# Optimization experiments

Hardware: AMD Instinct MI355X
Metric: run time of the kernel (lower is better)

The kernel has to match this reference:

```python
import jax, jax.numpy as jnp
import numpy as np

N = 131072      # octree nodes at this depth
C_IN = 256      # in_channels == out_channels
C_B = 64        # bottleneck channels = out_channels // 4
K = 27          # 3x3x3 octree kernel neighborhood
EPS = 1e-5


def _bn(x, g, b, m, v):
    # inference-style BatchNorm with given running stats
    return (x - m) * (g * jax.lax.rsqrt(v + EPS)) + b


def setup_inputs() -> dict:
    key = jax.random.key(0)
    ks = jax.random.split(key, 20)
    inp = {
        "data": jax.random.normal(ks[0], (N, C_IN), dtype=jnp.float32),
        "neigh": jax.random.randint(ks[1], (N, K), 0, N, dtype=jnp.int32),
        "depth": 6,
        # conv1x1a (Linear, no bias) + BN
        "w1": jax.random.normal(ks[2], (C_IN, C_B), dtype=jnp.float32) * 0.05,
        "bn1_g": jax.random.uniform(ks[3], (C_B,), dtype=jnp.float32) + 0.5,
        "bn1_b": jax.random.normal(ks[4], (C_B,), dtype=jnp.float32) * 0.1,
        "bn1_m": jax.random.normal(ks[5], (C_B,), dtype=jnp.float32) * 0.1,
        "bn1_v": jax.random.uniform(ks[6], (C_B,), dtype=jnp.float32) + 0.5,
        # octree conv3x3 (27-neighbor gather + GEMM, no bias) + BN
        "w3": jax.random.normal(ks[7], (K, C_B, C_B), dtype=jnp.float32) * 0.02,
        "bn2_g": jax.random.uniform(ks[8], (C_B,), dtype=jnp.float32) + 0.5,
        "bn2_b": jax.random.normal(ks[9], (C_B,), dtype=jnp.float32) * 0.1,
        "bn2_m": jax.random.normal(ks[10], (C_B,), dtype=jnp.float32) * 0.1,
        "bn2_v": jax.random.uniform(ks[11], (C_B,), dtype=jnp.float32) + 0.5,
        # conv1x1b + BN (no ReLU)
        "w2": jax.random.normal(ks[12], (C_B, C_IN), dtype=jnp.float32) * 0.05,
        "bn3_g": jax.random.uniform(ks[13], (C_IN,), dtype=jnp.float32) + 0.5,
        "bn3_b": jax.random.normal(ks[14], (C_IN,), dtype=jnp.float32) * 0.1,
        "bn3_m": jax.random.normal(ks[15], (C_IN,), dtype=jnp.float32) * 0.1,
        "bn3_v": jax.random.uniform(ks[16], (C_IN,), dtype=jnp.float32) + 0.5,
    }
    return inp


def reference(data, neigh, depth, w1, bn1_g, bn1_b, bn1_m, bn1_v,
              w3, bn2_g, bn2_b, bn2_m, bn2_v,
              w2, bn3_g, bn3_b, bn3_m, bn3_v):
    # conv1x1a + BN + ReLU
    c1 = jax.nn.relu(_bn(data @ w1, bn1_g, bn1_b, bn1_m, bn1_v))  # [N, C_B]
    # octree conv3x3: gather 27 neighbors then contract with [K, C_B, C_B]
    gathered = c1[neigh]                                          # [N, K, C_B]
    c2 = jnp.einsum('nkc,kcd->nd', gathered, w3)                  # [N, C_B]
    c2 = jax.nn.relu(_bn(c2, bn2_g, bn2_b, bn2_m, bn2_v))
    # conv1x1b + BN (no relu)
    c3 = _bn(c2 @ w2, bn3_g, bn3_b, bn3_m, bn3_v)                 # [N, C_IN]
    # residual (in_channels == out_channels -> identity shortcut) + ReLU
    return jax.nn.relu(c3 + data)
```

## Files before the change

### kernel.cpp

```cpp
#include <hip/hip_runtime.h>

#define NN 131072
#define CIN 256
#define CB 64
#define KNB 27

typedef __attribute__((ext_vector_type(8))) short short8_t;
typedef __attribute__((ext_vector_type(4))) float f32x4;

__device__ inline unsigned short f2bf(float f) {
    union { float f; unsigned u; } x; x.f = f;
    unsigned r = x.u + 0x7fffu + ((x.u >> 16) & 1u);
    return (unsigned short)(r >> 16);
}

__device__ inline f32x4 mfma16(short8_t a, short8_t b, f32x4 c) {
    return __builtin_amdgcn_mfma_f32_16x16x32_bf16(a, b, c, 0, 0, 0);
}

__global__ __launch_bounds__(256) void prep_kernel(
    const float* __restrict__ w1, const float* __restrict__ w3, const float* __restrict__ w2,
    const float* __restrict__ g1, const float* __restrict__ b1, const float* __restrict__ m1, const float* __restrict__ v1,
    const float* __restrict__ g2, const float* __restrict__ b2, const float* __restrict__ m2, const float* __restrict__ v2,
    const float* __restrict__ g3, const float* __restrict__ b3, const float* __restrict__ m3, const float* __restrict__ v3,
    unsigned short* __restrict__ w1p, unsigned short* __restrict__ w3p, unsigned short* __restrict__ w2p,
    float* __restrict__ bias1, float* __restrict__ bias2, float* __restrict__ bias3)
{
    int t = blockIdx.x * 256 + threadIdx.x;
    if (t < 16384) {
        int j = t & 7, lane = (t >> 3) & 63, tt = (t >> 9) & 3, s = t >> 11;
        int c = s * 32 + (lane >> 4) * 8 + j;
        int d = tt * 16 + (lane & 15);
        float sc = g1[d] * rsqrtf(v1[d] + 1e-5f);
        w1p[t] = f2bf(w1[c * CB + d] * sc);
    } else if (t < 16384 + 110592) {
        int u = t - 16384;
        int j = u & 7, lane = (u >> 3) & 63, tt = (u >> 9) & 3, s = (u >> 11) & 1, k = u >> 12;
        int c = s * 32 + (lane >> 4) * 8 + j;
        int d = tt * 16 + (lane & 15);
        float sc = g2[d] * rsqrtf(v2[d] + 1e-5f);
        w3p[u] = f2bf(w3[(k * CB + c) * CB + d] * sc);
    } else if (t < 143360) {
        int u = t - 126976;
        int j = u & 7, lane = (u >> 3) & 63, ct = (u >> 9) & 15, s = u >> 13;
        int c = s * 32 + (lane >> 4) * 8 + j;
        int d = ct * 16 + (lane & 15);
        float sc = g3[d] * rsqrtf(v3[d] + 1e-5f);
        w2p[u] = f2bf(w2[c * CIN + d] * sc);
    } else if (t < 143744) {
        int u = t - 143360;
        if (u < 64)       { float sc = g1[u] * rsqrtf(v1[u] + 1e-5f); bias1[u] = b1[u] - m1[u] * sc; }
        else if (u < 128) { int d = u - 64;  float sc = g2[d] * rsqrtf(v2[d] + 1e-5f); bias2[d] = b2[d] - m2[d] * sc; }
        else              { int d = u - 128; float sc = g3[d] * rsqrtf(v3[d] + 1e-5f); bias3[d] = b3[d] - m3[d] * sc; }
    }
}

__global__ __launch_bounds__(256) void k1_conv1x1a(
    const float* __restrict__ data, const unsigned short* __restrict__ w1p,
    const float* __restrict__ bias1, unsigned short* __restrict__ c1b)
{
    __shared__ short8_t w1s[2048];
    int tid = threadIdx.x;
    const short8_t* wsrc = (const short8_t*)w1p;
#pragma unroll
    for (int i = 0; i < 8; i++) w1s[tid + i * 256] = wsrc[tid + i * 256];

    int lane = tid & 63, wave = tid >> 6;
    int g = lane >> 4, r = lane & 15;
    int rowbase = blockIdx.x * 128 + wave * 32;
    f32x4 acc[2][4] = {};
    __syncthreads();

#pragma unroll
    for (int s = 0; s < 8; s++) {
        short8_t a[2];
#pragma unroll
        for (int sub = 0; sub < 2; sub++) {
            const float* ap = data + (size_t)(rowbase + sub * 16 + r) * CIN + s * 32 + g * 8;
            float4 f0 = *(const float4*)ap;
            float4 f1 = *(const float4*)(ap + 4);
            short8_t av;
            av[0] = (short)f2bf(f0.x); av[1] = (short)f2bf(f0.y);
            av[2] = (short)f2bf(f0.z); av[3] = (short)f2bf(f0.w);
            av[4] = (short)f2bf(f1.x); av[5] = (short)f2bf(f1.y);
            av[6] = (short)f2bf(f1.z); av[7] = (short)f2bf(f1.w);
            a[sub] = av;
        }
#pragma unroll
        for (int t = 0; t < 4; t++) {
            short8_t b = w1s[(s * 4 + t) * 64 + lane];
            acc[0][t] = mfma16(a[0], b, acc[0][t]);
            acc[1][t] = mfma16(a[1], b, acc[1][t]);
        }
    }

#pragma unroll
    for (int sub = 0; sub < 2; sub++)
#pragma unroll
        for (int t = 0; t < 4; t++) {
            int col = t * 16 + r;
            float bs = bias1[col];
#pragma unroll
            for (int i = 0; i < 4; i++) {
                int row = rowbase + sub * 16 + g * 4 + i;
                c1b[row * CB + col] = f2bf(fmaxf(acc[sub][t][i] + bs, 0.f));
            }
        }
}

__global__ __launch_bounds__(256) void k2_conv3x3(
    const unsigned short* __restrict__ c1b, const int* __restrict__ neigh,
    const unsigned short* __restrict__ w3p, const float* __restrict__ bias2,
    unsigned short* __restrict__ c2b)
{
    __shared__ short8_t w3s[512];
    int tid = threadIdx.x;
    int lane = tid & 63, wave = tid >> 6;
    int g = lane >> 4, r = lane & 15;
    int rowbase = blockIdx.x * 128 + wave * 32;
    int n0 = rowbase + r, n1 = rowbase + 16 + r;
    f32x4 acc[2][4] = {};

    for (int k = 0; k < KNB; k++) {
        __syncthreads();
        const short8_t* src = (const short8_t*)(w3p + k * 4096);
        w3s[tid]       = src[tid];
        w3s[tid + 256] = src[tid + 256];

        int idx0 = neigh[n0 * KNB + k];
        int idx1 = neigh[n1 * KNB + k];
        const short8_t* ap0 = (const short8_t*)(c1b + (size_t)idx0 * CB);
        const short8_t* ap1 = (const short8_t*)(c1b + (size_t)idx1 * CB);
        short8_t a0s0 = ap0[g], a0s1 = ap0[4 + g];
        short8_t a1s0 = ap1[g], a1s1 = ap1[4 + g];
        __syncthreads();

#pragma unroll
        for (int t = 0; t < 4; t++) {
            short8_t b0 = w3s[t * 64 + lane];
            short8_t b1 = w3s[(4 + t) * 64 + lane];
            acc[0][t] = mfma16(a0s0, b0, acc[0][t]);
            acc[1][t] = mfma16(a1s0, b0, acc[1][t]);
            acc[0][t] = mfma16(a0s1, b1, acc[0][t]);
            acc[1][t] = mfma16(a1s1, b1, acc[1][t]);
        }
    }

#pragma unroll
    for (int sub = 0; sub < 2; sub++)
#pragma unroll
        for (int t = 0; t < 4; t++) {
            int col = t * 16 + r;
            float bs = bias2[col];
#pragma unroll
            for (int i = 0; i < 4; i++) {
                int row = rowbase + sub * 16 + g * 4 + i;
                c2b[row * CB + col] = f2bf(fmaxf(acc[sub][t][i] + bs, 0.f));
            }
        }
}

__global__ __launch_bounds__(256) void k3_conv1x1b(
    const unsigned short* __restrict__ c2b, const unsigned short* __restrict__ w2p,
    const float* __restrict__ bias3, const float* __restrict__ data,
    float* __restrict__ out)
{
    __shared__ short8_t w2s[2048];
    int tid = threadIdx.x;
    const short8_t* wsrc = (const short8_t*)w2p;
#pragma unroll
    for (int i = 0; i < 8; i++) w2s[tid + i * 256] = wsrc[tid + i * 256];

    int lane = tid & 63, wave = tid >> 6;
    int g = lane >> 4, r = lane & 15;
    int rowbase = blockIdx.x * 64;

    short8_t a[4][2];
#pragma unroll
    for (int sub = 0; sub < 4; sub++) {
        const short8_t* ap = (const short8_t*)(c2b + (size_t)(rowbase + sub * 16 + r) * CB);
        a[sub][0] = ap[g];
        a[sub][1] = ap[4 + g];
    }
    f32x4 acc[4][4] = {};
    __syncthreads();

#pragma unroll
    for (int s = 0; s < 2; s++)
#pragma unroll
        for (int t = 0; t < 4; t++) {
            short8_t b = w2s[(s * 16 + wave * 4 + t) * 64 + lane];
#pragma unroll
            for (int sub = 0; sub < 4; sub++)
                acc[sub][t] = mfma16(a[sub][s], b, acc[sub][t]);
        }

#pragma unroll
    for (int sub = 0; sub < 4; sub++)
#pragma unroll
        for (int t = 0; t < 4; t++) {
            int col = (wave * 4 + t) * 16 + r;
            float bs = bias3[col];
#pragma unroll
            for (int i = 0; i < 4; i++) {
                int row = rowbase + sub * 16 + g * 4 + i;
                size_t o = (size_t)row * CIN + col;
                out[o] = fmaxf(acc[sub][t][i] + bs + data[o], 0.f);
            }
        }
}

extern "C" void kernel_launch(void* const* d_in, const int* in_sizes, int n_in,
                              void* d_out, int out_size, void* d_ws, size_t ws_size,
                              hipStream_t stream)
{
    const float* data = (const float*)d_in[0];
    const int* neigh  = (const int*)d_in[1];
    const float* w1 = (const float*)d_in[3];
    const float* g1 = (const float*)d_in[4];
    const float* b1 = (const float*)d_in[5];
    const float* m1 = (const float*)d_in[6];
    const float* v1 = (const float*)d_in[7];
    const float* w3 = (const float*)d_in[8];
    const float* g2 = (const float*)d_in[9];
    const float* b2 = (const float*)d_in[10];
    const float* m2 = (const float*)d_in[11];
    const float* v2 = (const float*)d_in[12];
    const float* w2 = (const float*)d_in[13];
    const float* g3 = (const float*)d_in[14];
    const float* b3 = (const float*)d_in[15];
    const float* m3 = (const float*)d_in[16];
    const float* v3 = (const float*)d_in[17];
    float* out = (float*)d_out;

    char* ws = (char*)d_ws;
    unsigned short* c1b = (unsigned short*)ws;
    unsigned short* c2b = (unsigned short*)(ws + 16777216);
    unsigned short* w1p = (unsigned short*)(ws + 33554432);
    unsigned short* w3p = (unsigned short*)(ws + 33554432 + 32768);
    unsigned short* w2p = (unsigned short*)(ws + 33554432 + 32768 + 221184);
    float* bias1 = (float*)(ws + 33554432 + 32768 + 221184 + 32768);
    float* bias2 = bias1 + 64;
    float* bias3 = bias1 + 128;

    int n = in_sizes[0] / CIN;

    hipLaunchKernelGGL(prep_kernel, dim3(562), dim3(256), 0, stream,
                       w1, w3, w2, g1, b1, m1, v1, g2, b2, m2, v2, g3, b3, m3, v3,
                       w1p, w3p, w2p, bias1, bias2, bias3);
    hipLaunchKernelGGL(k1_conv1x1a, dim3(n / 128), dim3(256), 0, stream, data, w1p, bias1, c1b);
    hipLaunchKernelGGL(k2_conv3x3,  dim3(n / 128), dim3(256), 0, stream, c1b, neigh, w3p, bias2, c2b);
    hipLaunchKernelGGL(k3_conv1x1b, dim3(n / 64),  dim3(256), 0, stream, c2b, w2p, bias3, data, out);
}
```

Baseline: 198.2 us.

## Software-pipeline conv3x3 gathers and coalesce conv1x1b residual epilogue via LDS

The 3x3 octree conv kernel now stages the block's neighbor indices in LDS once. It double-buffers the gathered activations and weight fragments in registers, loaded directly from global memory, so the loads for step k+1 overlap the MFMAs for step k and the two per-step barriers disappear. The conv1x1b kernel drops its LDS weight staging in favour of direct global loads, and routes its output through an LDS tile so the residual add and store use coalesced float4 accesses. The cost is higher register pressure in k2, which gets a launch-bounds occupancy hint, and more LDS use in k3.

After: 172.5 us. -13.0%, faster.

```diff
diff --git a/kernel.cpp b/kernel.cpp
--- a/kernel.cpp
+++ b/kernel.cpp
@@ -108,43 +108,69 @@
         }
 }
 
-__global__ __launch_bounds__(256) void k2_conv3x3(
+#define K2_MFMA(aX, bX) \
+    _Pragma("unroll") for (int t = 0; t < 4; t++) { \
+        acc[0][t] = mfma16(aX[0], bX[t],     acc[0][t]); \
+        acc[1][t] = mfma16(aX[2], bX[t],     acc[1][t]); \
+        acc[0][t] = mfma16(aX[1], bX[4 + t], acc[0][t]); \
+        acc[1][t] = mfma16(aX[3], bX[4 + t], acc[1][t]); \
+    }
+
+#define K2_BODY(aC, bC, ixC0, ixC1, aN, bN, ixN0, ixN1, k) \
+    { \
+        if ((k) < 26) { \
+            const short8_t* p0 = (const short8_t*)(c1b + (size_t)(ixN0) * CB); \
+            const short8_t* p1 = (const short8_t*)(c1b + (size_t)(ixN1) * CB); \
+            aN[0] = p0[g]; aN[1] = p0[4 + g]; aN[2] = p1[g]; aN[3] = p1[4 + g]; \
+            const short8_t* bp = bbase + ((k) + 1) * 512; \
+            _Pragma("unroll") for (int f = 0; f < 8; f++) bN[f] = bp[f * 64 + lane]; \
+        } \
+        if ((k) < 25) { ixC0 = nidx[lr0 * KNB + (k) + 2]; ixC1 = nidx[lr1 * KNB + (k) + 2]; } \
+        K2_MFMA(aC, bC) \
+    }
+
+__global__ __launch_bounds__(256, 3) void k2_conv3x3(
     const unsigned short* __restrict__ c1b, const int* __restrict__ neigh,
     const unsigned short* __restrict__ w3p, const float* __restrict__ bias2,
     unsigned short* __restrict__ c2b)
 {
-    __shared__ short8_t w3s[512];
+    __shared__ int nidx[128 * KNB];
     int tid = threadIdx.x;
+    int rowbase = blockIdx.x * 128;
+
+    const int4* nsrc = (const int4*)(neigh + (size_t)rowbase * KNB);
+#pragma unroll
+    for (int i = 0; i < 4; i++) {
+        int p = tid + i * 256;
+        if (p < 864) ((int4*)nidx)[p] = nsrc[p];
+    }
+
     int lane = tid & 63, wave = tid >> 6;
     int g = lane >> 4, r = lane & 15;
-    int rowbase = blockIdx.x * 128 + wave * 32;
-    int n0 = rowbase + r, n1 = rowbase + 16 + r;
+    int lr0 = wave * 32 + r, lr1 = lr0 + 16;
+    __syncthreads();
+
+    const short8_t* bbase = (const short8_t*)w3p;
     f32x4 acc[2][4] = {};
-
-    for (int k = 0; k < KNB; k++) {
-        __syncthreads();
-        const short8_t* src = (const short8_t*)(w3p + k * 4096);
-        w3s[tid]       = src[tid];
-        w3s[tid + 256] = src[tid + 256];
-
-        int idx0 = neigh[n0 * KNB + k];
-        int idx1 = neigh[n1 * KNB + k];
-        const short8_t* ap0 = (const short8_t*)(c1b + (size_t)idx0 * CB);
-        const short8_t* ap1 = (const short8_t*)(c1b + (size_t)idx1 * CB);
-        short8_t a0s0 = ap0[g], a0s1 = ap0[4 + g];
-        short8_t a1s0 = ap1[g], a1s1 = ap1[4 + g];
-        __syncthreads();
-
-#pragma unroll
-        for (int t = 0; t < 4; t++) {
-            short8_t b0 = w3s[t * 64 + lane];
-            short8_t b1 = w3s[(4 + t) * 64 + lane];
-            acc[0][t] = mfma16(a0s0, b0, acc[0][t]);
-            acc[1][t] = mfma16(a1s0, b0, acc[1][t]);
-            acc[0][t] = mfma16(a0s1, b1, acc[0][t]);
-            acc[1][t] = mfma16(a1s1, b1, acc[1][t]);
-        }
-    }
+    short8_t aA[4], aB[4], bA[8], bB[8];
+    int ixA0, ixA1, ixB0, ixB1;
+
+    ixA0 = nidx[lr0 * KNB + 0]; ixA1 = nidx[lr1 * KNB + 0];
+    ixB0 = nidx[lr0 * KNB + 1]; ixB1 = nidx[lr1 * KNB + 1];
+    {
+        const short8_t* p0 = (const short8_t*)(c1b + (size_t)ixA0 * CB);
+        const short8_t* p1 = (const short8_t*)(c1b + (size_t)ixA1 * CB);
+        aA[0] = p0[g]; aA[1] = p0[4 + g]; aA[2] = p1[g]; aA[3] = p1[4 + g];
+#pragma unroll
+        for (int f = 0; f < 8; f++) bA[f] = bbase[f * 64 + lane];
+    }
+
+    for (int kk = 0; kk < 13; kk++) {
+        int k0 = kk * 2;
+        K2_BODY(aA, bA, ixA0, ixA1, aB, bB, ixB0, ixB1, k0)
+        K2_BODY(aB, bB, ixB0, ixB1, aA, bA, ixA0, ixA1, k0 + 1)
+    }
+    K2_BODY(aA, bA, ixA0, ixA1, aB, bB, ixB0, ixB1, 26)
 
 #pragma unroll
     for (int sub = 0; sub < 2; sub++)
@@ -154,7 +180,7 @@
             float bs = bias2[col];
 #pragma unroll
             for (int i = 0; i < 4; i++) {
-                int row = rowbase + sub * 16 + g * 4 + i;
+                int row = rowbase + wave * 32 + sub * 16 + g * 4 + i;
                 c2b[row * CB + col] = f2bf(fmaxf(acc[sub][t][i] + bs, 0.f));
             }
         }
@@ -165,16 +191,13 @@
     const float* __restrict__ bias3, const float* __restrict__ data,
     float* __restrict__ out)
 {
-    __shared__ short8_t w2s[2048];
+    __shared__ float otile[64 * 260];
     int tid = threadIdx.x;
-    const short8_t* wsrc = (const short8_t*)w2p;
-#pragma unroll
-    for (int i = 0; i < 8; i++) w2s[tid + i * 256] = wsrc[tid + i * 256];
-
     int lane = tid & 63, wave = tid >> 6;
     int g = lane >> 4, r = lane & 15;
     int rowbase = blockIdx.x * 64;
 
+    const short8_t* bbase = (const short8_t*)w2p;
     short8_t a[4][2];
 #pragma unroll
     for (int sub = 0; sub < 4; sub++) {
@@ -183,13 +206,11 @@
         a[sub][1] = ap[4 + g];
     }
     f32x4 acc[4][4] = {};
-    __syncthreads();
-
 #pragma unroll
     for (int s = 0; s < 2; s++)
 #pragma unroll
         for (int t = 0; t < 4; t++) {
-            short8_t b = w2s[(s * 16 + wave * 4 + t) * 64 + lane];
+            short8_t b = bbase[(s * 16 + wave * 4 + t) * 64 + lane];
 #pragma unroll
             for (int sub = 0; sub < 4; sub++)
                 acc[sub][t] = mfma16(a[sub][s], b, acc[sub][t]);
@@ -203,11 +224,27 @@
             float bs = bias3[col];
 #pragma unroll
             for (int i = 0; i < 4; i++) {
-                int row = rowbase + sub * 16 + g * 4 + i;
-                size_t o = (size_t)row * CIN + col;
-                out[o] = fmaxf(acc[sub][t][i] + bs + data[o], 0.f);
+                int row = sub * 16 + g * 4 + i;
+                otile[row * 260 + col] = acc[sub][t][i] + bs;
             }
         }
+    __syncthreads();
+
+    const float* dsrc = data + (size_t)rowbase * CIN;
+    float* dst = out + (size_t)rowbase * CIN;
+#pragma unroll
+    for (int p = 0; p < 16; p++) {
+        int flat = p * 1024 + tid * 4;
+        int row = flat >> 8, col = flat & 255;
+        float4 dv = *(const float4*)(dsrc + flat);
+        float4 ov = *(const float4*)(&otile[row * 260 + col]);
+        float4 res;
+        res.x = fmaxf(ov.x + dv.x, 0.f);
+        res.y = fmaxf(ov.y + dv.y, 0.f);
+        res.z = fmaxf(ov.z + dv.z, 0.f);
+        res.w = fmaxf(ov.w + dv.w, 0.f);
+        *(float4*)(dst + flat) = res;
+    }
 }
 
 extern "C" void kernel_launch(void* const* d_in, const int* in_sizes, int n_in,
@@ -224,8 +261,8 @@
     const float* w3 = (const float*)d_in[8];
     const float* g2 = (const float*)d_in[9];
     const float* b2 = (const float*)d_in[10];
+    const float* v2 = (const float*)d_in[12];
     const float* m2 = (const float*)d_in[11];
-    const float* v2 = (const float*)d_in[12];
     const float* w2 = (const float*)d_in[13];
     const float* g3 = (const float*)d_in[14];
     const float* b3 = (const float*)d_in[15];
```
